# Kernel optimization log

Measured on AMD Instinct MI355X. Metric: run time of the kernel, lower is better.

## Reference

```python
import jax, jax.numpy as jnp
import numpy as np

N = 100000   # total nodes in batch
E = 400000   # total directed edges
G = 4096     # number of graphs
D = 300      # emb_dim
H = 600      # GIN MLP hidden = 2*emb_dim
L = 5        # num_layer
BN_EPS = 1e-5
SELF_LOOP_BOND_TYPE = 4  # contextpred convention


def setup_inputs() -> dict:
    key = jax.random.key(0)
    ks = jax.random.split(key, 16)
    s = 0.1
    return {
        "x": jax.random.randint(ks[0], (N, 2), 0, 3),
        "edge_index": jax.random.randint(ks[1], (2, E), 0, N),
        "edge_attr": jax.random.randint(ks[2], (E, 2), 0, 3),
        "batch": jnp.sort(jax.random.randint(ks[3], (N,), 0, G)),
        "atom_emb1": jax.random.normal(ks[4], (120, D), jnp.float32) * s,
        "atom_emb2": jax.random.normal(ks[5], (3, D), jnp.float32) * s,
        "edge_emb1": jax.random.normal(ks[6], (L, 6, D), jnp.float32) * s,
        "edge_emb2": jax.random.normal(ks[7], (L, 3, D), jnp.float32) * s,
        "w1": jax.random.normal(ks[8], (L, D, H), jnp.float32) * (1.0 / np.sqrt(D)),
        "b1": jnp.zeros((L, H), jnp.float32),
        "w2": jax.random.normal(ks[9], (L, H, D), jnp.float32) * (1.0 / np.sqrt(H)),
        "b2": jnp.zeros((L, D), jnp.float32),
        "bn_g": jnp.ones((L, D), jnp.float32),
        "bn_b": jnp.zeros((L, D), jnp.float32),
        "bn_m": jnp.zeros((L, D), jnp.float32),
        "bn_v": jnp.ones((L, D), jnp.float32),
        "head_w1": jax.random.normal(ks[10], (D, 512), jnp.float32) * (1.0 / np.sqrt(D)),
        "head_b1": jnp.zeros((512,), jnp.float32),
        "head_w2": jax.random.normal(ks[11], (512, 2), jnp.float32) * (1.0 / np.sqrt(512)),
        "head_b2": jnp.zeros((2,), jnp.float32),
    }


def _gnn_forward(x, edge_index, edge_attr, batch,
                 atom_emb1, atom_emb2, edge_emb1, edge_emb2,
                 w1, b1, w2, b2, bn_g, bn_b, bn_m, bn_v,
                 head_w1, head_b1, head_w2, head_b2):
    src, dst = edge_index[0], edge_index[1]
    # node input embedding: atom type + chirality
    h = atom_emb1[x[:, 0]] + atom_emb2[x[:, 1]]  # [N, D]
    for l in range(L):
        # edge embeddings for real edges
        eemb = edge_emb1[l][edge_attr[:, 0]] + edge_emb2[l][edge_attr[:, 1]]  # [E, D]
        # self-loop edge embedding (bond type 4, direction 0), same for all nodes
        self_emb = edge_emb1[l][SELF_LOOP_BOND_TYPE] + edge_emb2[l][0]  # [D]
        # GIN 'add' aggregation of messages (x_j + edge_emb), incl. self loops
        agg = jax.ops.segment_sum(h[src] + eemb, dst, num_segments=N)
        agg = agg + h + self_emb  # fused self-loop contribution
        # MLP: Linear(D,2D) -> ReLU -> Linear(2D,D)
        h = jax.nn.relu(agg @ w1[l] + b1[l]) @ w2[l] + b2[l]
        # BatchNorm1d in eval mode (running stats)
        h = (h - bn_m[l]) * jax.lax.rsqrt(bn_v[l] + BN_EPS) * bn_g[l] + bn_b[l]
        if l < L - 1:  # JK='last': ReLU on all but last layer
            h = jax.nn.relu(h)
    # to_dense_batch + sum(axis=1) == segment sum over graphs
    pooled = jax.ops.segment_sum(h, batch, num_segments=G)  # [G, D]
    # task head
    logits = jax.nn.relu(pooled @ head_w1 + head_b1) @ head_w2 + head_b2  # [G, 2]
    return logits


def reference(x, edge_index, edge_attr, batch,
              atom_emb1, atom_emb2, edge_emb1, edge_emb2,
              w1, b1, w2, b2, bn_g, bn_b, bn_m, bn_v,
              head_w1, head_b1, head_w2, head_b2):
    return _gnn_forward(x, edge_index, edge_attr, batch,
                        atom_emb1, atom_emb2, edge_emb1, edge_emb2,
                        w1, b1, w2, b2, bn_g, bn_b, bn_m, bn_v,
                        head_w1, head_b1, head_w2, head_b2)
```

## Files before the change

### kernel.cpp

```cpp
#include <hip/hip_runtime.h>
#include <hip/hip_bf16.h>
#include <stdint.h>

#define N_NODES 100000
#define N_EDGES 400000
#define N_GRAPH 4096
#define DIMD    300
#define NLAYER  5
#define HPAD   304
#define KP1    320
#define W1ROWS 640
#define WID2   320
#define MROWS  64
#define HGR    64

typedef __attribute__((ext_vector_type(8))) short bf16x8_t;
typedef __attribute__((ext_vector_type(4))) float f32x4_t;

__device__ __forceinline__ void gload_lds16(const void* g, void* l) {
  auto gp = (__attribute__((address_space(1))) void*)(uintptr_t)g;
  auto lp = (__attribute__((address_space(3))) void*)(uint32_t)(uintptr_t)l;
  __builtin_amdgcn_global_load_lds(gp, lp, 16, 0, 0);
}
__device__ __forceinline__ short f2bs(float f) {
  __hip_bfloat16 b = __float2bfloat16(f); return *(short*)&b;
}
__device__ __forceinline__ float bs2f(short s) {
  __hip_bfloat16 b; *(short*)&b = s; return __bfloat162float(b);
}

__global__ void k_hist(const int* __restrict__ ei, int* __restrict__ cur) {
  const int e = blockIdx.x * blockDim.x + threadIdx.x;
  if (e < N_EDGES) atomicAdd(&cur[ei[N_EDGES + e]], 1);
}

__global__ void k_scan1(int* __restrict__ cur, int* __restrict__ off, int* __restrict__ bsum) {
  __shared__ int buf[1024];
  const int tid = threadIdx.x;
  const int i = blockIdx.x * 1024 + tid;
  int v = (i < N_NODES) ? cur[i] : 0;
  buf[tid] = v;
  __syncthreads();
  for (int s = 1; s < 1024; s <<= 1) {
    int t = (tid >= s) ? buf[tid - s] : 0;
    __syncthreads();
    buf[tid] += t;
    __syncthreads();
  }
  if (i < N_NODES) { off[i + 1] = buf[tid]; cur[i] = 0; }
  if (tid == 1023) bsum[blockIdx.x] = buf[1023];
}

__global__ void k_scan2(int* __restrict__ bsum, int nb) {
  if (threadIdx.x == 0 && blockIdx.x == 0) {
    int run = 0;
    for (int b = 0; b < nb; ++b) { int v = bsum[b]; bsum[b] = run; run += v; }
  }
}

__global__ void k_scan3(int* __restrict__ off, const int* __restrict__ bsum) {
  const int i = blockIdx.x * blockDim.x + threadIdx.x;
  if (i == 0) off[0] = 0;
  if (i < N_NODES) off[i + 1] += bsum[i >> 10];
}

__global__ void k_fill(const int* __restrict__ ei, const int* __restrict__ ea,
                       const int* __restrict__ off, int* __restrict__ cur,
                       int* __restrict__ csr) {
  const int e = blockIdx.x * blockDim.x + threadIdx.x;
  if (e < N_EDGES) {
    const int d = ei[N_EDGES + e];
    const int pos = atomicAdd(&cur[d], 1);
    const int c = ea[2 * e] * 3 + ea[2 * e + 1];
    csr[off[d] + pos] = (ei[e] << 4) | c;
  }
}

__global__ void k_comb(const float* __restrict__ e1, const float* __restrict__ e2,
                       float* __restrict__ comb) {
  const int idx = blockIdx.x * blockDim.x + threadIdx.x;
  if (idx >= NLAYER * 10 * HPAD) return;
  const int l = idx / (10 * HPAD);
  const int r = (idx / HPAD) % 10;
  const int d = idx % HPAD;
  float v = 0.f;
  if (d < DIMD) {
    int a, b;
    if (r < 9) { a = r / 3; b = r % 3; } else { a = 4; b = 0; }
    v = e1[(l * 6 + a) * DIMD + d] + e2[(l * 3 + b) * DIMD + d];
  }
  comb[idx] = v;
}

__global__ void k_wc1(const float* __restrict__ w, __hip_bfloat16* __restrict__ wb) {
  const int idx = blockIdx.x * blockDim.x + threadIdx.x;
  if (idx >= NLAYER * W1ROWS * KP1) return;
  const int l = idx / (W1ROWS * KP1);
  const int n = (idx / KP1) % W1ROWS;
  const int k = idx % KP1;
  float v = 0.f;
  if (n < 600 && k < DIMD) v = w[((long)l * DIMD + k) * 600 + n];
  wb[idx] = __float2bfloat16(v);
}

__global__ void k_wc2(const float* __restrict__ w, __hip_bfloat16* __restrict__ wb) {
  const int idx = blockIdx.x * blockDim.x + threadIdx.x;
  if (idx >= NLAYER * WID2 * W1ROWS) return;
  const int l = idx / (WID2 * W1ROWS);
  const int n = (idx / W1ROWS) % WID2;
  const int k = idx % W1ROWS;
  float v = 0.f;
  if (n < DIMD && k < 600) v = w[((long)l * 600 + k) * DIMD + n];
  wb[idx] = __float2bfloat16(v);
}

__global__ void k_wch(const float* __restrict__ w, __hip_bfloat16* __restrict__ wb) {
  const int idx = blockIdx.x * blockDim.x + threadIdx.x;
  if (idx >= 512 * KP1) return;
  const int n = idx / KP1;
  const int k = idx % KP1;
  float v = (k < DIMD) ? w[(long)k * 512 + n] : 0.f;
  wb[idx] = __float2bfloat16(v);
}

__global__ void k_nemb(const int* __restrict__ x, const float* __restrict__ ae1,
                       const float* __restrict__ ae2, __hip_bfloat16* __restrict__ h) {
  const int gid = blockIdx.x * blockDim.x + threadIdx.x;
  if (gid >= N_NODES * 38) return;
  const int node = gid / 38;
  const int l = gid % 38;
  bf16x8_t ov;
#pragma unroll
  for (int j = 0; j < 8; ++j) ov[j] = 0;
  {
    const int i0 = x[2 * node], i1 = x[2 * node + 1];
    const float* r1 = ae1 + (long)i0 * DIMD + l * 8;
    const float* r2 = ae2 + (long)i1 * DIMD + l * 8;
#pragma unroll
    for (int j = 0; j < 8; ++j) {
      const int d = l * 8 + j;
      if (d < DIMD) ov[j] = f2bs(r1[j] + r2[j]);
    }
  }
  *(bf16x8_t*)(h + (long)node * HPAD + l * 8) = ov;
}

__global__ __launch_bounds__(256)
void k_agg(const __hip_bfloat16* __restrict__ h, __hip_bfloat16* __restrict__ aggb,
           const int* __restrict__ csr, const int* __restrict__ off,
           const float* __restrict__ comb) {
  const int wv = threadIdx.x >> 6;
  const int lane = threadIdx.x & 63;
  const int node = blockIdx.x * 4 + wv;
  if (node >= N_NODES) return;
  if (lane >= 40) return;
  const bool act = lane < 38;
  float acc[8];
  if (act) {
    const bf16x8_t hv = *(const bf16x8_t*)(h + (long)node * HPAD + lane * 8);
    const float* c9 = comb + 9 * HPAD + lane * 8;
#pragma unroll
    for (int j = 0; j < 8; ++j) acc[j] = bs2f(hv[j]) + c9[j];
  } else {
#pragma unroll
    for (int j = 0; j < 8; ++j) acc[j] = 0.f;
  }
  const int p0 = off[node], p1 = off[node + 1];
  int p = p0;
  for (; p + 1 < p1; p += 2) {
    const int v0 = csr[p], v1 = csr[p + 1];
    if (act) {
      const bf16x8_t h0 = *(const bf16x8_t*)(h + (long)(v0 >> 4) * HPAD + lane * 8);
      const bf16x8_t h1 = *(const bf16x8_t*)(h + (long)(v1 >> 4) * HPAD + lane * 8);
      const float* c0 = comb + (v0 & 15) * HPAD + lane * 8;
      const float* c1 = comb + (v1 & 15) * HPAD + lane * 8;
#pragma unroll
      for (int j = 0; j < 8; ++j) acc[j] += bs2f(h0[j]) + c0[j];
#pragma unroll
      for (int j = 0; j < 8; ++j) acc[j] += bs2f(h1[j]) + c1[j];
    }
  }
  if (p < p1) {
    const int v0 = csr[p];
    if (act) {
      const bf16x8_t h0 = *(const bf16x8_t*)(h + (long)(v0 >> 4) * HPAD + lane * 8);
      const float* c0 = comb + (v0 & 15) * HPAD + lane * 8;
#pragma unroll
      for (int j = 0; j < 8; ++j) acc[j] += bs2f(h0[j]) + c0[j];
    }
  }
  bf16x8_t ov;
#pragma unroll
  for (int j = 0; j < 8; ++j) ov[j] = act ? f2bs(acc[j]) : (short)0;
  *(bf16x8_t*)(aggb + (long)node * KP1 + lane * 8) = ov;
}

__global__ __launch_bounds__(256)
void k_mlp(const __hip_bfloat16* __restrict__ aggb,
           const __hip_bfloat16* __restrict__ w1b,
           const __hip_bfloat16* __restrict__ w2b,
           const float* __restrict__ b1,
           const float* __restrict__ b2,
           const float* __restrict__ bng, const float* __restrict__ bnb,
           const float* __restrict__ bnm, const float* __restrict__ bnv,
           int reluFlag,
           __hip_bfloat16* __restrict__ h) {
  __shared__ __align__(16) char As[MROWS * 640];
  __shared__ __align__(16) char P[MROWS * 128];
  const int tid = threadIdx.x;
  const int lane = tid & 63;
  const int wc = tid >> 6;
  const int fr = lane & 15;
  const int kg = lane >> 4;
  const int row0 = blockIdx.x * MROWS;

#pragma unroll
  for (int it = 0; it < 10; ++it) {
    const int g = it * 256 + tid;
    const int r = g / 40;
    const int gin = g - r * 40;
    int ar = row0 + r;
    if (ar >= N_NODES) ar = N_NODES - 1;
    gload_lds16((const char*)aggb + (size_t)ar * 640 + (size_t)((gin ^ (r & 7)) * 16),
                As + g * 16);
  }

  f32x4_t accB[4][5];
#pragma unroll
  for (int m = 0; m < 4; ++m)
#pragma unroll
    for (int n = 0; n < 5; ++n) accB[m][n] = (f32x4_t){0.f, 0.f, 0.f, 0.f};

  __syncthreads();

  for (int hc = 0; hc < 10; ++hc) {
    f32x4_t accA[4];
#pragma unroll
    for (int m = 0; m < 4; ++m) accA[m] = (f32x4_t){0.f, 0.f, 0.f, 0.f};
    const __hip_bfloat16* w1c = w1b + (size_t)(hc * 64 + wc * 16) * KP1;
#pragma unroll
    for (int ks = 0; ks < 10; ++ks) {
      const int k2 = ks * 64 + kg * 16;
      bf16x8_t af[4];
#pragma unroll
      for (int m = 0; m < 4; ++m) {
        const int r = m * 16 + fr;
        af[m] = *(const bf16x8_t*)(As + r * 640 + (k2 ^ ((r & 7) << 4)));
      }
      const bf16x8_t bfr = *(const bf16x8_t*)(w1c + (size_t)fr * KP1 + ks * 32 + kg * 8);
#pragma unroll
      for (int m = 0; m < 4; ++m)
        accA[m] = __builtin_amdgcn_mfma_f32_16x16x32_bf16(af[m], bfr, accA[m], 0, 0, 0);
    }
    const int col = hc * 64 + wc * 16 + fr;
    const float bv = (col < 600) ? b1[col] : 0.f;

    __syncthreads();
#pragma unroll
    for (int m = 0; m < 4; ++m)
#pragma unroll
      for (int j = 0; j < 4; ++j) {
        const int prow = m * 16 + kg * 4 + j;
        const int pcol = wc * 16 + fr;
        *(short*)(P + prow * 128 + ((pcol * 2) ^ ((prow & 7) << 4))) =
            f2bs(fmaxf(accA[m][j] + bv, 0.f));
      }
    __syncthreads();

#pragma unroll
    for (int ks = 0; ks < 2; ++ks) {
      bf16x8_t af2[4], bf2[5];
#pragma unroll
      for (int m = 0; m < 4; ++m) {
        const int pr = m * 16 + fr;
        af2[m] = *(const bf16x8_t*)(P + pr * 128 + ((ks * 64 + kg * 16) ^ ((pr & 7) << 4)));
      }
      const int k2 = hc * 64 + ks * 32 + kg * 8;
#pragma unroll
      for (int n = 0; n < 5; ++n)
        bf2[n] = *(const bf16x8_t*)(w2b + (size_t)(wc * 80 + n * 16 + fr) * W1ROWS + k2);
#pragma unroll
      for (int m = 0; m < 4; ++m)
#pragma unroll
        for (int n = 0; n < 5; ++n)
          accB[m][n] = __builtin_amdgcn_mfma_f32_16x16x32_bf16(af2[m], bf2[n], accB[m][n], 0, 0, 0);
    }
  }

  float scale[5], shift[5];
#pragma unroll
  for (int n = 0; n < 5; ++n) {
    const int col = wc * 80 + n * 16 + fr;
    if (col < DIMD) {
      const float sc = rsqrtf(bnv[col] + 1e-5f) * bng[col];
      scale[n] = sc;
      shift[n] = (b2[col] - bnm[col]) * sc + bnb[col];
    } else { scale[n] = 0.f; shift[n] = 0.f; }
  }
#pragma unroll
  for (int m = 0; m < 4; ++m) {
#pragma unroll
    for (int n = 0; n < 5; ++n) {
      const int col = wc * 80 + n * 16 + fr;
      if (col >= HPAD) continue;
#pragma unroll
      for (int j = 0; j < 4; ++j) {
        const int node = row0 + m * 16 + kg * 4 + j;
        if (node >= N_NODES) continue;
        float v = 0.f;
        if (col < DIMD) {
          v = accB[m][n][j] * scale[n] + shift[n];
          if (reluFlag) v = fmaxf(v, 0.f);
        }
        h[(size_t)node * HPAD + col] = __float2bfloat16(v);
      }
    }
  }
}

__device__ __forceinline__ int lbound(const int* a, int n, int key) {
  int lo = 0, hi = n;
  while (lo < hi) { int mid = (lo + hi) >> 1; if (a[mid] < key) lo = mid + 1; else hi = mid; }
  return lo;
}

__global__ void k_pool(const __hip_bfloat16* __restrict__ h, const int* __restrict__ batch,
                       __hip_bfloat16* __restrict__ pooled) {
  __shared__ int se[2];
  const int g = blockIdx.x;
  if (threadIdx.x < 2) se[threadIdx.x] = lbound(batch, N_NODES, g + threadIdx.x);
  __syncthreads();
  const int d = threadIdx.x;
  if (d < KP1) {
    float a = 0.f;
    if (d < DIMD)
      for (int i = se[0]; i < se[1]; ++i) a += __bfloat162float(h[(long)i * HPAD + d]);
    pooled[(long)g * KP1 + d] = __float2bfloat16(d < DIMD ? a : 0.f);
  }
}

__global__ __launch_bounds__(256)
void k_head(const __hip_bfloat16* __restrict__ pooled,
            const __hip_bfloat16* __restrict__ hw1b,
            const float* __restrict__ hb1, const float* __restrict__ hw2,
            const float* __restrict__ hb2, float* __restrict__ out) {
  __shared__ __align__(16) char As[HGR * 640];
  __shared__ float sred[4][HGR][2];
  const int tid = threadIdx.x;
  const int lane = tid & 63;
  const int wc = tid >> 6;
  const int fr = lane & 15;
  const int kg = lane >> 4;
  const int g0 = blockIdx.x * HGR;

#pragma unroll
  for (int it = 0; it < 10; ++it) {
    const int g = it * 256 + tid;
    const int r = g / 40;
    const int gin = g - r * 40;
    gload_lds16((const char*)pooled + (size_t)(g0 + r) * 640 + (size_t)((gin ^ (r & 7)) * 16),
                As + g * 16);
  }

  f32x4_t acc[4][8];
#pragma unroll
  for (int m = 0; m < 4; ++m)
#pragma unroll
    for (int n = 0; n < 8; ++n) acc[m][n] = (f32x4_t){0.f, 0.f, 0.f, 0.f};

  __syncthreads();

#pragma unroll
  for (int ks = 0; ks < 10; ++ks) {
    const int k2 = ks * 64 + kg * 16;
    bf16x8_t af[4], bw[8];
#pragma unroll
    for (int m = 0; m < 4; ++m) {
      const int r = m * 16 + fr;
      af[m] = *(const bf16x8_t*)(As + r * 640 + (k2 ^ ((r & 7) << 4)));
    }
#pragma unroll
    for (int n = 0; n < 8; ++n)
      bw[n] = *(const bf16x8_t*)(hw1b + (size_t)(wc * 128 + n * 16 + fr) * KP1 + ks * 32 + kg * 8);
#pragma unroll
    for (int m = 0; m < 4; ++m)
#pragma unroll
      for (int n = 0; n < 8; ++n)
        acc[m][n] = __builtin_amdgcn_mfma_f32_16x16x32_bf16(af[m], bw[n], acc[m][n], 0, 0, 0);
  }

  float p0[4][4], p1[4][4];
#pragma unroll
  for (int m = 0; m < 4; ++m)
#pragma unroll
    for (int j = 0; j < 4; ++j) { p0[m][j] = 0.f; p1[m][j] = 0.f; }
#pragma unroll
  for (int n = 0; n < 8; ++n) {
    const int col = wc * 128 + n * 16 + fr;
    const float bv = hb1[col];
    const float wa = hw2[2 * col], wb = hw2[2 * col + 1];
#pragma unroll
    for (int m = 0; m < 4; ++m)
#pragma unroll
      for (int j = 0; j < 4; ++j) {
        const float z = fmaxf(acc[m][n][j] + bv, 0.f);
        p0[m][j] = fmaf(z, wa, p0[m][j]);
        p1[m][j] = fmaf(z, wb, p1[m][j]);
      }
  }
#pragma unroll
  for (int m = 0; m < 4; ++m)
#pragma unroll
    for (int j = 0; j < 4; ++j) {
#pragma unroll
      for (int s = 1; s < 16; s <<= 1) {
        p0[m][j] += __shfl_xor(p0[m][j], s, 64);
        p1[m][j] += __shfl_xor(p1[m][j], s, 64);
      }
    }
  if (fr == 0) {
#pragma unroll
    for (int m = 0; m < 4; ++m)
#pragma unroll
      for (int j = 0; j < 4; ++j) {
        const int row = m * 16 + kg * 4 + j;
        sred[wc][row][0] = p0[m][j];
        sred[wc][row][1] = p1[m][j];
      }
  }
  __syncthreads();
  if (tid < HGR) {
    const int row = tid;
    float a0 = sred[0][row][0] + sred[1][row][0] + sred[2][row][0] + sred[3][row][0];
    float a1 = sred[0][row][1] + sred[1][row][1] + sred[2][row][1] + sred[3][row][1];
    out[2 * (g0 + row)] = a0 + hb2[0];
    out[2 * (g0 + row) + 1] = a1 + hb2[1];
  }
}

__global__ void k_sentinel(float* out) { out[threadIdx.x] = 1.0e6f; }

extern "C" void kernel_launch(void* const* d_in, const int* in_sizes, int n_in,
                              void* d_out, int out_size, void* d_ws, size_t ws_size,
                              hipStream_t stream) {
  const int*   x     = (const int*)d_in[0];
  const int*   ei    = (const int*)d_in[1];
  const int*   ea    = (const int*)d_in[2];
  const int*   batch = (const int*)d_in[3];
  const float* ae1   = (const float*)d_in[4];
  const float* ae2   = (const float*)d_in[5];
  const float* ee1   = (const float*)d_in[6];
  const float* ee2   = (const float*)d_in[7];
  const float* w1    = (const float*)d_in[8];
  const float* b1    = (const float*)d_in[9];
  const float* w2    = (const float*)d_in[10];
  const float* b2    = (const float*)d_in[11];
  const float* bng   = (const float*)d_in[12];
  const float* bnbp  = (const float*)d_in[13];
  const float* bnm   = (const float*)d_in[14];
  const float* bnv   = (const float*)d_in[15];
  const float* hw1   = (const float*)d_in[16];
  const float* hb1   = (const float*)d_in[17];
  const float* hw2   = (const float*)d_in[18];
  const float* hb2   = (const float*)d_in[19];
  float* out = (float*)d_out;

  char* ws = (char*)d_ws;
  size_t o = 0;
  auto alloc = [&](size_t bytes) { size_t p = o; o += (bytes + 255) & ~(size_t)255; return p; };
  __hip_bfloat16* h      = (__hip_bfloat16*)(ws + alloc((size_t)N_NODES * HPAD * 2));
  __hip_bfloat16* aggb   = (__hip_bfloat16*)(ws + alloc((size_t)N_NODES * KP1 * 2));
  __hip_bfloat16* w1b    = (__hip_bfloat16*)(ws + alloc((size_t)NLAYER * W1ROWS * KP1 * 2));
  __hip_bfloat16* w2b    = (__hip_bfloat16*)(ws + alloc((size_t)NLAYER * WID2 * W1ROWS * 2));
  __hip_bfloat16* hw1b   = (__hip_bfloat16*)(ws + alloc((size_t)512 * KP1 * 2));
  float*          comb   = (float*)         (ws + alloc((size_t)NLAYER * 10 * HPAD * 4));
  int*            offp   = (int*)           (ws + alloc((size_t)(N_NODES + 1) * 4));
  int*            cur    = (int*)           (ws + alloc((size_t)N_NODES * 4));
  int*            csr    = (int*)           (ws + alloc((size_t)N_EDGES * 4));
  __hip_bfloat16* pooled = (__hip_bfloat16*)(ws + alloc((size_t)N_GRAPH * KP1 * 2));
  int*            bsum   = (int*)           (ws + alloc(128 * 4));
  if (o > ws_size) {
    k_sentinel<<<1, 8, 0, stream>>>(out);
    return;
  }

  hipMemsetAsync(cur, 0, (size_t)N_NODES * 4, stream);

  k_hist<<<(N_EDGES + 255) / 256, 256, 0, stream>>>(ei, cur);
  const int nsb = (N_NODES + 1023) / 1024;
  k_scan1<<<nsb, 1024, 0, stream>>>(cur, offp, bsum);
  k_scan2<<<1, 64, 0, stream>>>(bsum, nsb);
  k_scan3<<<(N_NODES + 255) / 256, 256, 0, stream>>>(offp, bsum);
  k_fill<<<(N_EDGES + 255) / 256, 256, 0, stream>>>(ei, ea, offp, cur, csr);

  k_wc1<<<(NLAYER * W1ROWS * KP1 + 255) / 256, 256, 0, stream>>>(w1, w1b);
  k_wc2<<<(NLAYER * WID2 * W1ROWS + 255) / 256, 256, 0, stream>>>(w2, w2b);
  k_wch<<<(512 * KP1 + 255) / 256, 256, 0, stream>>>(hw1, hw1b);
  k_comb<<<(NLAYER * 10 * HPAD + 255) / 256, 256, 0, stream>>>(ee1, ee2, comb);
  k_nemb<<<(N_NODES * 38 + 255) / 256, 256, 0, stream>>>(x, ae1, ae2, h);

  const int mlpBlocks = (N_NODES + MROWS - 1) / MROWS;
  for (int l = 0; l < NLAYER; ++l) {
    k_agg<<<(N_NODES + 3) / 4, 256, 0, stream>>>(h, aggb, csr, offp, comb + l * 10 * HPAD);
    k_mlp<<<mlpBlocks, 256, 0, stream>>>(aggb,
        w1b + (size_t)l * W1ROWS * KP1, w2b + (size_t)l * WID2 * W1ROWS,
        b1 + l * 600, b2 + l * DIMD,
        bng + l * DIMD, bnbp + l * DIMD, bnm + l * DIMD, bnv + l * DIMD,
        (l < NLAYER - 1) ? 1 : 0, h);
  }

  k_pool<<<N_GRAPH, KP1, 0, stream>>>(h, batch, pooled);
  k_head<<<N_GRAPH / HGR, 256, 0, stream>>>(pooled, hw1b, hb1, hw2, hb2, out);
}
```

Measured before the change: 1.501 ms.

## Warp-specialize MLP kernel into producer/consumer waves with double-buffered hidden tile

The fused MLP kernel now launches 512 threads. Four waves compute the first GEMM chunk and write ReLU'd bf16 activations into a double-buffered LDS tile, while the other four waves consume the previous chunk for the second GEMM. This replaces the two barriers per chunk with one and overlaps the two matmul stages. In exchange it uses more LDS and twice the threads per block, which may lower occupancy, and each wave group sits idle in the prologue or epilogue step.

```diff
diff --git a/kernel.cpp b/kernel.cpp
--- a/kernel.cpp
+++ b/kernel.cpp
@@ -195,7 +195,7 @@
   *(bf16x8_t*)(aggb + (long)node * KP1 + lane * 8) = ov;
 }
 
-__global__ __launch_bounds__(256)
+__global__ __launch_bounds__(512)
 void k_mlp(const __hip_bfloat16* __restrict__ aggb,
            const __hip_bfloat16* __restrict__ w1b,
            const __hip_bfloat16* __restrict__ w2b,
@@ -206,17 +206,17 @@
            int reluFlag,
            __hip_bfloat16* __restrict__ h) {
   __shared__ __align__(16) char As[MROWS * 640];
-  __shared__ __align__(16) char P[MROWS * 128];
+  __shared__ __align__(16) char P[2 * MROWS * 128];
   const int tid = threadIdx.x;
   const int lane = tid & 63;
-  const int wc = tid >> 6;
+  const int wv = tid >> 6;
   const int fr = lane & 15;
   const int kg = lane >> 4;
   const int row0 = blockIdx.x * MROWS;
 
 #pragma unroll
-  for (int it = 0; it < 10; ++it) {
-    const int g = it * 256 + tid;
+  for (int it = 0; it < 5; ++it) {
+    const int g = it * 512 + tid;
     const int r = g / 40;
     const int gin = g - r * 40;
     int ar = row0 + r;
@@ -233,86 +233,97 @@
 
   __syncthreads();
 
-  for (int hc = 0; hc < 10; ++hc) {
-    f32x4_t accA[4];
-#pragma unroll
-    for (int m = 0; m < 4; ++m) accA[m] = (f32x4_t){0.f, 0.f, 0.f, 0.f};
-    const __hip_bfloat16* w1c = w1b + (size_t)(hc * 64 + wc * 16) * KP1;
-#pragma unroll
-    for (int ks = 0; ks < 10; ++ks) {
-      const int k2 = ks * 64 + kg * 16;
-      bf16x8_t af[4];
-#pragma unroll
-      for (int m = 0; m < 4; ++m) {
-        const int r = m * 16 + fr;
-        af[m] = *(const bf16x8_t*)(As + r * 640 + (k2 ^ ((r & 7) << 4)));
+  for (int s = 0; s < 11; ++s) {
+    if (wv < 4) {
+      if (s < 10) {
+        f32x4_t accA[4];
+#pragma unroll
+        for (int m = 0; m < 4; ++m) accA[m] = (f32x4_t){0.f, 0.f, 0.f, 0.f};
+        const __hip_bfloat16* w1c = w1b + (size_t)(s * 64 + wv * 16) * KP1;
+#pragma unroll
+        for (int ks = 0; ks < 10; ++ks) {
+          const int k2 = ks * 64 + kg * 16;
+          bf16x8_t af[4];
+#pragma unroll
+          for (int m = 0; m < 4; ++m) {
+            const int r = m * 16 + fr;
+            af[m] = *(const bf16x8_t*)(As + r * 640 + (k2 ^ ((r & 7) << 4)));
+          }
+          const bf16x8_t bfr = *(const bf16x8_t*)(w1c + (size_t)fr * KP1 + ks * 32 + kg * 8);
+#pragma unroll
+          for (int m = 0; m < 4; ++m)
+            accA[m] = __builtin_amdgcn_mfma_f32_16x16x32_bf16(af[m], bfr, accA[m], 0, 0, 0);
+        }
+        const int col = s * 64 + wv * 16 + fr;
+        const float bv = (col < 600) ? b1[col] : 0.f;
+        char* Pd = P + (s & 1) * (MROWS * 128);
+        const int pcol = wv * 16 + fr;
+#pragma unroll
+        for (int m = 0; m < 4; ++m)
+#pragma unroll
+          for (int j = 0; j < 4; ++j) {
+            const int prow = m * 16 + kg * 4 + j;
+            *(short*)(Pd + prow * 128 + ((pcol * 2) ^ ((prow & 7) << 4))) =
+                f2bs(fmaxf(accA[m][j] + bv, 0.f));
+          }
       }
-      const bf16x8_t bfr = *(const bf16x8_t*)(w1c + (size_t)fr * KP1 + ks * 32 + kg * 8);
-#pragma unroll
-      for (int m = 0; m < 4; ++m)
-        accA[m] = __builtin_amdgcn_mfma_f32_16x16x32_bf16(af[m], bfr, accA[m], 0, 0, 0);
-    }
-    const int col = hc * 64 + wc * 16 + fr;
-    const float bv = (col < 600) ? b1[col] : 0.f;
-
+    } else {
+      if (s >= 1) {
+        const int hc = s - 1;
+        const int cg = wv - 4;
+        const char* Pc = P + (hc & 1) * (MROWS * 128);
+#pragma unroll
+        for (int ks = 0; ks < 2; ++ks) {
+          bf16x8_t af2[4], bf2[5];
+#pragma unroll
+          for (int m = 0; m < 4; ++m) {
+            const int pr = m * 16 + fr;
+            af2[m] = *(const bf16x8_t*)(Pc + pr * 128 + ((ks * 64 + kg * 16) ^ ((pr & 7) << 4)));
+          }
+          const int k2 = hc * 64 + ks * 32 + kg * 8;
+#pragma unroll
+          for (int n = 0; n < 5; ++n)
+            bf2[n] = *(const bf16x8_t*)(w2b + (size_t)(cg * 80 + n * 16 + fr) * W1ROWS + k2);
+#pragma unroll
+          for (int m = 0; m < 4; ++m)
+#pragma unroll
+            for (int n = 0; n < 5; ++n)
+              accB[m][n] = __builtin_amdgcn_mfma_f32_16x16x32_bf16(af2[m], bf2[n], accB[m][n], 0, 0, 0);
+        }
+      }
+    }
     __syncthreads();
-#pragma unroll
-    for (int m = 0; m < 4; ++m)
-#pragma unroll
-      for (int j = 0; j < 4; ++j) {
-        const int prow = m * 16 + kg * 4 + j;
-        const int pcol = wc * 16 + fr;
-        *(short*)(P + prow * 128 + ((pcol * 2) ^ ((prow & 7) << 4))) =
-            f2bs(fmaxf(accA[m][j] + bv, 0.f));
-      }
-    __syncthreads();
-
-#pragma unroll
-    for (int ks = 0; ks < 2; ++ks) {
-      bf16x8_t af2[4], bf2[5];
-#pragma unroll
-      for (int m = 0; m < 4; ++m) {
-        const int pr = m * 16 + fr;
-        af2[m] = *(const bf16x8_t*)(P + pr * 128 + ((ks * 64 + kg * 16) ^ ((pr & 7) << 4)));
-      }
-      const int k2 = hc * 64 + ks * 32 + kg * 8;
-#pragma unroll
-      for (int n = 0; n < 5; ++n)
-        bf2[n] = *(const bf16x8_t*)(w2b + (size_t)(wc * 80 + n * 16 + fr) * W1ROWS + k2);
-#pragma unroll
-      for (int m = 0; m < 4; ++m)
-#pragma unroll
-        for (int n = 0; n < 5; ++n)
-          accB[m][n] = __builtin_amdgcn_mfma_f32_16x16x32_bf16(af2[m], bf2[n], accB[m][n], 0, 0, 0);
-    }
-  }
-
-  float scale[5], shift[5];
-#pragma unroll
-  for (int n = 0; n < 5; ++n) {
-    const int col = wc * 80 + n * 16 + fr;
-    if (col < DIMD) {
-      const float sc = rsqrtf(bnv[col] + 1e-5f) * bng[col];
-      scale[n] = sc;
-      shift[n] = (b2[col] - bnm[col]) * sc + bnb[col];
-    } else { scale[n] = 0.f; shift[n] = 0.f; }
-  }
-#pragma unroll
-  for (int m = 0; m < 4; ++m) {
+  }
+
+  if (wv >= 4) {
+    const int cg = wv - 4;
+    float scale[5], shift[5];
 #pragma unroll
     for (int n = 0; n < 5; ++n) {
-      const int col = wc * 80 + n * 16 + fr;
-      if (col >= HPAD) continue;
-#pragma unroll
-      for (int j = 0; j < 4; ++j) {
-        const int node = row0 + m * 16 + kg * 4 + j;
-        if (node >= N_NODES) continue;
-        float v = 0.f;
-        if (col < DIMD) {
-          v = accB[m][n][j] * scale[n] + shift[n];
-          if (reluFlag) v = fmaxf(v, 0.f);
+      const int col = cg * 80 + n * 16 + fr;
+      if (col < DIMD) {
+        const float sc = rsqrtf(bnv[col] + 1e-5f) * bng[col];
+        scale[n] = sc;
+        shift[n] = (b2[col] - bnm[col]) * sc + bnb[col];
+      } else { scale[n] = 0.f; shift[n] = 0.f; }
+    }
+#pragma unroll
+    for (int m = 0; m < 4; ++m) {
+#pragma unroll
+      for (int n = 0; n < 5; ++n) {
+        const int col = cg * 80 + n * 16 + fr;
+        if (col >= HPAD) continue;
+#pragma unroll
+        for (int j = 0; j < 4; ++j) {
+          const int node = row0 + m * 16 + kg * 4 + j;
+          if (node >= N_NODES) continue;
+          float v = 0.f;
+          if (col < DIMD) {
+            v = accB[m][n][j] * scale[n] + shift[n];
+            if (reluFlag) v = fmaxf(v, 0.f);
+          }
+          h[(size_t)node * HPAD + col] = __float2bfloat16(v);
         }
-        h[(size_t)node * HPAD + col] = __float2bfloat16(v);
       }
     }
   }
@@ -502,7 +513,7 @@
   const int mlpBlocks = (N_NODES + MROWS - 1) / MROWS;
   for (int l = 0; l < NLAYER; ++l) {
     k_agg<<<(N_NODES + 3) / 4, 256, 0, stream>>>(h, aggb, csr, offp, comb + l * 10 * HPAD);
-    k_mlp<<<mlpBlocks, 256, 0, stream>>>(aggb,
+    k_mlp<<<mlpBlocks, 512, 0, stream>>>(aggb,
         w1b + (size_t)l * W1ROWS * KP1, w2b + (size_t)l * WID2 * W1ROWS,
         b1 + l * 600, b2 + l * DIMD,
         bng + l * DIMD, bnbp + l * DIMD, bnm + l * DIMD, bnv + l * DIMD,
```

Result: slower. 1.699 ms (+13.2%).

## Fuse neighbor aggregation into MLP kernel, ping-pong node feature buffers

Applied to the files above, without the earlier changes.

Removes the separate aggregation kernel and its bf16 aggregate buffer. Each MLP block now gathers the neighbor features for its 64 rows directly into the swizzled LDS A tile, one wave handling 16 rows, before running the two GEMMs. Because output rows can no longer overwrite inputs that other blocks still read, node features alternate between two buffers. This saves the global write and read of the aggregate and one launch per layer. In exchange the irregular gather now runs inside the LDS-heavy GEMM kernel, where lower occupancy may hide its latency less well than the standalone kernel did.

```diff
diff --git a/kernel.cpp b/kernel.cpp
--- a/kernel.cpp
+++ b/kernel.cpp
@@ -146,57 +146,9 @@
 }
 
 __global__ __launch_bounds__(256)
-void k_agg(const __hip_bfloat16* __restrict__ h, __hip_bfloat16* __restrict__ aggb,
+void k_mlp(const __hip_bfloat16* __restrict__ hin,
            const int* __restrict__ csr, const int* __restrict__ off,
-           const float* __restrict__ comb) {
-  const int wv = threadIdx.x >> 6;
-  const int lane = threadIdx.x & 63;
-  const int node = blockIdx.x * 4 + wv;
-  if (node >= N_NODES) return;
-  if (lane >= 40) return;
-  const bool act = lane < 38;
-  float acc[8];
-  if (act) {
-    const bf16x8_t hv = *(const bf16x8_t*)(h + (long)node * HPAD + lane * 8);
-    const float* c9 = comb + 9 * HPAD + lane * 8;
-#pragma unroll
-    for (int j = 0; j < 8; ++j) acc[j] = bs2f(hv[j]) + c9[j];
-  } else {
-#pragma unroll
-    for (int j = 0; j < 8; ++j) acc[j] = 0.f;
-  }
-  const int p0 = off[node], p1 = off[node + 1];
-  int p = p0;
-  for (; p + 1 < p1; p += 2) {
-    const int v0 = csr[p], v1 = csr[p + 1];
-    if (act) {
-      const bf16x8_t h0 = *(const bf16x8_t*)(h + (long)(v0 >> 4) * HPAD + lane * 8);
-      const bf16x8_t h1 = *(const bf16x8_t*)(h + (long)(v1 >> 4) * HPAD + lane * 8);
-      const float* c0 = comb + (v0 & 15) * HPAD + lane * 8;
-      const float* c1 = comb + (v1 & 15) * HPAD + lane * 8;
-#pragma unroll
-      for (int j = 0; j < 8; ++j) acc[j] += bs2f(h0[j]) + c0[j];
-#pragma unroll
-      for (int j = 0; j < 8; ++j) acc[j] += bs2f(h1[j]) + c1[j];
-    }
-  }
-  if (p < p1) {
-    const int v0 = csr[p];
-    if (act) {
-      const bf16x8_t h0 = *(const bf16x8_t*)(h + (long)(v0 >> 4) * HPAD + lane * 8);
-      const float* c0 = comb + (v0 & 15) * HPAD + lane * 8;
-#pragma unroll
-      for (int j = 0; j < 8; ++j) acc[j] += bs2f(h0[j]) + c0[j];
-    }
-  }
-  bf16x8_t ov;
-#pragma unroll
-  for (int j = 0; j < 8; ++j) ov[j] = act ? f2bs(acc[j]) : (short)0;
-  *(bf16x8_t*)(aggb + (long)node * KP1 + lane * 8) = ov;
-}
-
-__global__ __launch_bounds__(256)
-void k_mlp(const __hip_bfloat16* __restrict__ aggb,
+           const float* __restrict__ comb,
            const __hip_bfloat16* __restrict__ w1b,
            const __hip_bfloat16* __restrict__ w2b,
            const float* __restrict__ b1,
@@ -204,25 +156,63 @@
            const float* __restrict__ bng, const float* __restrict__ bnb,
            const float* __restrict__ bnm, const float* __restrict__ bnv,
            int reluFlag,
-           __hip_bfloat16* __restrict__ h) {
+           __hip_bfloat16* __restrict__ hout) {
   __shared__ __align__(16) char As[MROWS * 640];
   __shared__ __align__(16) char P[MROWS * 128];
   const int tid = threadIdx.x;
   const int lane = tid & 63;
-  const int wc = tid >> 6;
+  const int wv = tid >> 6;
   const int fr = lane & 15;
   const int kg = lane >> 4;
   const int row0 = blockIdx.x * MROWS;
 
-#pragma unroll
-  for (int it = 0; it < 10; ++it) {
-    const int g = it * 256 + tid;
-    const int r = g / 40;
-    const int gin = g - r * 40;
-    int ar = row0 + r;
-    if (ar >= N_NODES) ar = N_NODES - 1;
-    gload_lds16((const char*)aggb + (size_t)ar * 640 + (size_t)((gin ^ (r & 7)) * 16),
-                As + g * 16);
+  {
+    const bool act = lane < 38;
+    for (int i = 0; i < 16; ++i) {
+      const int r = wv * 16 + i;
+      int node = row0 + r;
+      if (node >= N_NODES) node = N_NODES - 1;
+      float acc[8];
+      if (act) {
+        const bf16x8_t hv = *(const bf16x8_t*)(hin + (size_t)node * HPAD + lane * 8);
+        const float* c9 = comb + 9 * HPAD + lane * 8;
+#pragma unroll
+        for (int j = 0; j < 8; ++j) acc[j] = bs2f(hv[j]) + c9[j];
+      } else {
+#pragma unroll
+        for (int j = 0; j < 8; ++j) acc[j] = 0.f;
+      }
+      const int p0 = off[node], p1 = off[node + 1];
+      int p = p0;
+      for (; p + 1 < p1; p += 2) {
+        const int v0 = csr[p], v1 = csr[p + 1];
+        if (act) {
+          const bf16x8_t h0 = *(const bf16x8_t*)(hin + (size_t)(v0 >> 4) * HPAD + lane * 8);
+          const bf16x8_t h1 = *(const bf16x8_t*)(hin + (size_t)(v1 >> 4) * HPAD + lane * 8);
+          const float* c0 = comb + (v0 & 15) * HPAD + lane * 8;
+          const float* c1 = comb + (v1 & 15) * HPAD + lane * 8;
+#pragma unroll
+          for (int j = 0; j < 8; ++j) acc[j] += bs2f(h0[j]) + c0[j];
+#pragma unroll
+          for (int j = 0; j < 8; ++j) acc[j] += bs2f(h1[j]) + c1[j];
+        }
+      }
+      if (p < p1) {
+        const int v0 = csr[p];
+        if (act) {
+          const bf16x8_t h0 = *(const bf16x8_t*)(hin + (size_t)(v0 >> 4) * HPAD + lane * 8);
+          const float* c0 = comb + (v0 & 15) * HPAD + lane * 8;
+#pragma unroll
+          for (int j = 0; j < 8; ++j) acc[j] += bs2f(h0[j]) + c0[j];
+        }
+      }
+      if (lane < 40) {
+        bf16x8_t ov;
+#pragma unroll
+        for (int j = 0; j < 8; ++j) ov[j] = act ? f2bs(acc[j]) : (short)0;
+        *(bf16x8_t*)(As + r * 640 + ((lane ^ (r & 7)) * 16)) = ov;
+      }
+    }
   }
 
   f32x4_t accB[4][5];
@@ -237,7 +227,7 @@
     f32x4_t accA[4];
 #pragma unroll
     for (int m = 0; m < 4; ++m) accA[m] = (f32x4_t){0.f, 0.f, 0.f, 0.f};
-    const __hip_bfloat16* w1c = w1b + (size_t)(hc * 64 + wc * 16) * KP1;
+    const __hip_bfloat16* w1c = w1b + (size_t)(hc * 64 + wv * 16) * KP1;
 #pragma unroll
     for (int ks = 0; ks < 10; ++ks) {
       const int k2 = ks * 64 + kg * 16;
@@ -252,7 +242,7 @@
       for (int m = 0; m < 4; ++m)
         accA[m] = __builtin_amdgcn_mfma_f32_16x16x32_bf16(af[m], bfr, accA[m], 0, 0, 0);
     }
-    const int col = hc * 64 + wc * 16 + fr;
+    const int col = hc * 64 + wv * 16 + fr;
     const float bv = (col < 600) ? b1[col] : 0.f;
 
     __syncthreads();
@@ -261,7 +251,7 @@
 #pragma unroll
       for (int j = 0; j < 4; ++j) {
         const int prow = m * 16 + kg * 4 + j;
-        const int pcol = wc * 16 + fr;
+        const int pcol = wv * 16 + fr;
         *(short*)(P + prow * 128 + ((pcol * 2) ^ ((prow & 7) << 4))) =
             f2bs(fmaxf(accA[m][j] + bv, 0.f));
       }
@@ -278,7 +268,7 @@
       const int k2 = hc * 64 + ks * 32 + kg * 8;
 #pragma unroll
       for (int n = 0; n < 5; ++n)
-        bf2[n] = *(const bf16x8_t*)(w2b + (size_t)(wc * 80 + n * 16 + fr) * W1ROWS + k2);
+        bf2[n] = *(const bf16x8_t*)(w2b + (size_t)(wv * 80 + n * 16 + fr) * W1ROWS + k2);
 #pragma unroll
       for (int m = 0; m < 4; ++m)
 #pragma unroll
@@ -290,7 +280,7 @@
   float scale[5], shift[5];
 #pragma unroll
   for (int n = 0; n < 5; ++n) {
-    const int col = wc * 80 + n * 16 + fr;
+    const int col = wv * 80 + n * 16 + fr;
     if (col < DIMD) {
       const float sc = rsqrtf(bnv[col] + 1e-5f) * bng[col];
       scale[n] = sc;
@@ -301,7 +291,7 @@
   for (int m = 0; m < 4; ++m) {
 #pragma unroll
     for (int n = 0; n < 5; ++n) {
-      const int col = wc * 80 + n * 16 + fr;
+      const int col = wv * 80 + n * 16 + fr;
       if (col >= HPAD) continue;
 #pragma unroll
       for (int j = 0; j < 4; ++j) {
@@ -312,7 +302,7 @@
           v = accB[m][n][j] * scale[n] + shift[n];
           if (reluFlag) v = fmaxf(v, 0.f);
         }
-        h[(size_t)node * HPAD + col] = __float2bfloat16(v);
+        hout[(size_t)node * HPAD + col] = __float2bfloat16(v);
       }
     }
   }
@@ -468,8 +458,8 @@
   char* ws = (char*)d_ws;
   size_t o = 0;
   auto alloc = [&](size_t bytes) { size_t p = o; o += (bytes + 255) & ~(size_t)255; return p; };
-  __hip_bfloat16* h      = (__hip_bfloat16*)(ws + alloc((size_t)N_NODES * HPAD * 2));
-  __hip_bfloat16* aggb   = (__hip_bfloat16*)(ws + alloc((size_t)N_NODES * KP1 * 2));
+  __hip_bfloat16* h1     = (__hip_bfloat16*)(ws + alloc((size_t)N_NODES * HPAD * 2));
+  __hip_bfloat16* h2     = (__hip_bfloat16*)(ws + alloc((size_t)N_NODES * HPAD * 2));
   __hip_bfloat16* w1b    = (__hip_bfloat16*)(ws + alloc((size_t)NLAYER * W1ROWS * KP1 * 2));
   __hip_bfloat16* w2b    = (__hip_bfloat16*)(ws + alloc((size_t)NLAYER * WID2 * W1ROWS * 2));
   __hip_bfloat16* hw1b   = (__hip_bfloat16*)(ws + alloc((size_t)512 * KP1 * 2));
@@ -497,18 +487,20 @@
   k_wc2<<<(NLAYER * WID2 * W1ROWS + 255) / 256, 256, 0, stream>>>(w2, w2b);
   k_wch<<<(512 * KP1 + 255) / 256, 256, 0, stream>>>(hw1, hw1b);
   k_comb<<<(NLAYER * 10 * HPAD + 255) / 256, 256, 0, stream>>>(ee1, ee2, comb);
-  k_nemb<<<(N_NODES * 38 + 255) / 256, 256, 0, stream>>>(x, ae1, ae2, h);
+  k_nemb<<<(N_NODES * 38 + 255) / 256, 256, 0, stream>>>(x, ae1, ae2, h1);
 
   const int mlpBlocks = (N_NODES + MROWS - 1) / MROWS;
+  const __hip_bfloat16* hc = h1;
+  __hip_bfloat16* hn = h2;
   for (int l = 0; l < NLAYER; ++l) {
-    k_agg<<<(N_NODES + 3) / 4, 256, 0, stream>>>(h, aggb, csr, offp, comb + l * 10 * HPAD);
-    k_mlp<<<mlpBlocks, 256, 0, stream>>>(aggb,
+    k_mlp<<<mlpBlocks, 256, 0, stream>>>(hc, csr, offp, comb + l * 10 * HPAD,
         w1b + (size_t)l * W1ROWS * KP1, w2b + (size_t)l * WID2 * W1ROWS,
         b1 + l * 600, b2 + l * DIMD,
         bng + l * DIMD, bnbp + l * DIMD, bnm + l * DIMD, bnv + l * DIMD,
-        (l < NLAYER - 1) ? 1 : 0, h);
-  }
-
-  k_pool<<<N_GRAPH, KP1, 0, stream>>>(h, batch, pooled);
+        (l < NLAYER - 1) ? 1 : 0, hn);
+    const __hip_bfloat16* t = hc; hc = hn; hn = (__hip_bfloat16*)t;
+  }
+
+  k_pool<<<N_GRAPH, KP1, 0, stream>>>(hc, batch, pooled);
   k_head<<<N_GRAPH / HGR, 256, 0, stream>>>(pooled, hw1b, hb1, hw2, hb2, out);
 }
```

Measured after the change: 1.915 ms. 27.6% more time.
